# Kernel optimization log

Measured on AMD Instinct MI355X. Metric: run time of the kernel, lower is better.

The kernel has to match this reference:

```python
import jax, jax.numpy as jnp
import numpy as np

B, S, D, H, E, K = 4, 2048, 1024, 2048, 8, 2
GH = max(D // 2, 32)  # 512 gating hidden


def setup_inputs() -> dict:
    key = jax.random.key(0)
    ks = jax.random.split(key, 16)
    def xav(k, shape):
        fan_in, fan_out = shape[0], shape[1]
        lim = (6.0 / (fan_in + fan_out)) ** 0.5
        return jax.random.uniform(k, shape, jnp.float32, -lim, lim)
    return {
        'x': jax.random.normal(ks[0], (B, S, D), jnp.float32),
        'feature_types': jax.random.randint(ks[1], (B, S), 0, 3),
        'gw1': xav(ks[2], (D, GH)), 'gb1': jnp.zeros((GH,), jnp.float32),
        'gw2': xav(ks[3], (GH, GH // 2)), 'gb2': jnp.zeros((GH // 2,), jnp.float32),
        'gw3': xav(ks[4], (GH // 2, E)), 'gb3': jnp.zeros((E,), jnp.float32),
        'type_emb': jax.random.normal(ks[5], (3, GH // 4), jnp.float32),
        'tw': xav(ks[6], (GH // 4, E)), 'tb': jnp.zeros((E,), jnp.float32),
        'ew': jax.random.normal(ks[7], (E, D, H), jnp.float32) * (1.0 / D ** 0.5),
        'eb': jnp.zeros((E, H), jnp.float32),
        'ow': xav(ks[8], (H, D)), 'ob': jnp.zeros((D,), jnp.float32),
    }


def reference(x, feature_types, gw1, gb1, gw2, gb2, gw3, gb3, type_emb, tw, tb, ew, eb, ow, ob):
    # Gating network (eval mode: dropout = identity)
    h = jax.nn.relu(x @ gw1 + gb1)
    h = jax.nn.relu(h @ gw2 + gb2)
    gate_logits = h @ gw3 + gb3                      # [B,S,E]
    type_bias = type_emb[feature_types] @ tw + tb    # [B,S,E]
    gate_weights = jax.nn.softmax(gate_logits + type_bias, axis=-1)

    # Top-k routing, renormalize selected weights
    expert_weights, expert_indices = jax.lax.top_k(gate_weights, K)  # [B,S,K]
    expert_weights = expert_weights / expert_weights.sum(-1, keepdims=True)

    # Dense expert compute (faithful to original: every expert on every token)
    expert_outputs = jnp.einsum('bsd,edh->bseh', x, ew) + eb         # [B,S,E,H]

    # Gather selected experts and combine
    sel = jnp.take_along_axis(expert_outputs, expert_indices[..., None], axis=2)  # [B,S,K,H]
    output = jnp.sum(expert_weights[..., None] * sel, axis=2)        # [B,S,H]

    output = jax.nn.relu(output)
    return output @ ow + ob                                          # [B,S,D]
```

## Files before the change

### kernel.cpp

```cpp
#include <hip/hip_runtime.h>

#define T_TOK 8192
#define DDIM 1024
#define GH1 512
#define GH2 256
#define NEXP 8
#define HDIM 2048

typedef __attribute__((ext_vector_type(8))) short short8;
typedef __attribute__((ext_vector_type(4))) float f32x4;

__device__ __forceinline__ unsigned short f2bf(float f) {
    unsigned int u = __float_as_uint(f);
    u += 0x7fffu + ((u >> 16) & 1u);
    return (unsigned short)(u >> 16);
}
__device__ __forceinline__ float bf2f(unsigned short h) {
    return __uint_as_float(((unsigned int)h) << 16);
}

__device__ __forceinline__ void async16(const void* g, void* l) {
#if __has_builtin(__builtin_amdgcn_global_load_lds)
    __builtin_amdgcn_global_load_lds((const __attribute__((address_space(1))) void*)g,
                                     (__attribute__((address_space(3))) void*)l, 16, 0, 0);
#else
    *(uint4*)l = *(const uint4*)g;
#endif
}

__global__ __launch_bounds__(256)
void f2b_kernel(const float* __restrict__ in, unsigned short* __restrict__ out)
{
    size_t i = ((size_t)blockIdx.x * 256 + threadIdx.x) * 8;
    float4 a = *(const float4*)(in + i);
    float4 b = *(const float4*)(in + i + 4);
    uint4 r;
    r.x = (unsigned)f2bf(a.x) | ((unsigned)f2bf(a.y) << 16);
    r.y = (unsigned)f2bf(a.z) | ((unsigned)f2bf(a.w) << 16);
    r.z = (unsigned)f2bf(b.x) | ((unsigned)f2bf(b.y) << 16);
    r.w = (unsigned)f2bf(b.z) | ((unsigned)f2bf(b.w) << 16);
    *(uint4*)(out + i) = r;
}

__global__ __launch_bounds__(256)
void transpose_f2b(const float* __restrict__ in, unsigned short* __restrict__ out,
                   int R, int C, int tilesC, int ntile)
{
    int bid = blockIdx.x;
    int z = bid / ntile;
    int r = bid - z * ntile;
    int tr = r / tilesC, tc = r - tr * tilesC;
    const float* ib = in + (size_t)z * R * C;
    unsigned short* ob = out + (size_t)z * R * C;
    __shared__ float lds[32][33];
    int t = threadIdx.x;
    int i = t >> 3, j4 = (t & 7) << 2;
    float4 v = *(const float4*)(ib + (size_t)(tr * 32 + i) * C + tc * 32 + j4);
    lds[i][j4 + 0] = v.x;
    lds[i][j4 + 1] = v.y;
    lds[i][j4 + 2] = v.z;
    lds[i][j4 + 3] = v.w;
    __syncthreads();
    ushort4 o;
    o.x = f2bf(lds[j4 + 0][i]);
    o.y = f2bf(lds[j4 + 1][i]);
    o.z = f2bf(lds[j4 + 2][i]);
    o.w = f2bf(lds[j4 + 3][i]);
    *(ushort4*)(ob + (size_t)(tc * 32 + i) * R + tr * 32 + j4) = o;
}

__global__ __launch_bounds__(256)
void sgemm_relu(const float* __restrict__ A, const float* __restrict__ B,
                const float* __restrict__ bias, float* __restrict__ C,
                int N, int Kd, int nbn)
{
    int bid = blockIdx.x;
    int bm = bid / nbn, bn = bid - bm * nbn;
    __shared__ float As[16 * 128];
    __shared__ float Bs[16 * 128];
    int t = threadIdx.x;
    int tx = t & 15, ty = t >> 4;
    float acc[8][8];
#pragma unroll
    for (int i = 0; i < 8; ++i)
#pragma unroll
        for (int j = 0; j < 8; ++j) acc[i][j] = 0.f;

    for (int k0 = 0; k0 < Kd; k0 += 16) {
        __syncthreads();
#pragma unroll
        for (int c = 0; c < 2; ++c) {
            int idx = t + c * 256;
            int row = idx >> 2, kk = (idx & 3) << 2;
            float4 v = *(const float4*)(A + (size_t)(bm * 128 + row) * Kd + k0 + kk);
            As[(kk + 0) * 128 + row] = v.x;
            As[(kk + 1) * 128 + row] = v.y;
            As[(kk + 2) * 128 + row] = v.z;
            As[(kk + 3) * 128 + row] = v.w;
            int kk2 = idx >> 5, n2 = (idx & 31) << 2;
            *(float4*)&Bs[kk2 * 128 + n2] =
                *(const float4*)(B + (size_t)(k0 + kk2) * N + bn * 128 + n2);
        }
        __syncthreads();
#pragma unroll
        for (int kk = 0; kk < 16; ++kk) {
            float a[8], b[8];
            *(float4*)&a[0] = *(const float4*)&As[kk * 128 + ty * 8];
            *(float4*)&a[4] = *(const float4*)&As[kk * 128 + ty * 8 + 4];
            *(float4*)&b[0] = *(const float4*)&Bs[kk * 128 + tx * 8];
            *(float4*)&b[4] = *(const float4*)&Bs[kk * 128 + tx * 8 + 4];
#pragma unroll
            for (int i = 0; i < 8; ++i)
#pragma unroll
                for (int j = 0; j < 8; ++j)
                    acc[i][j] = fmaf(a[i], b[j], acc[i][j]);
        }
    }
#pragma unroll
    for (int i = 0; i < 8; ++i) {
        int row = bm * 128 + ty * 8 + i;
#pragma unroll
        for (int j = 0; j < 8; ++j) {
            int col = bn * 128 + tx * 8 + j;
            float v = acc[i][j] + bias[col];
            C[(size_t)row * N + col] = v > 0.f ? v : 0.f;
        }
    }
}

__global__ __launch_bounds__(256)
void gate_tail(const float* __restrict__ h2, const int* __restrict__ ftyp,
               const float* __restrict__ gw3, const float* __restrict__ gb3,
               const float* __restrict__ temb, const float* __restrict__ tw,
               const float* __restrict__ tb,
               int* __restrict__ eidx, float* __restrict__ ewt)
{
    __shared__ float sw3[GH2 * NEXP];
    __shared__ float stw[128 * NEXP];
    __shared__ float ste[3 * 128];
    int t = threadIdx.x;
    for (int i = t; i < GH2 * NEXP; i += 256) sw3[i] = gw3[i];
    for (int i = t; i < 128 * NEXP; i += 256) stw[i] = tw[i];
    for (int i = t; i < 3 * 128; i += 256) ste[i] = temb[i];
    __syncthreads();
    int tok = blockIdx.x * 256 + t;
    float lg[NEXP];
#pragma unroll
    for (int e = 0; e < NEXP; ++e) lg[e] = gb3[e] + tb[e];
    const float* hrow = h2 + (size_t)tok * GH2;
    for (int k = 0; k < GH2; k += 4) {
        float4 hv = *(const float4*)(hrow + k);
        float hvv[4] = {hv.x, hv.y, hv.z, hv.w};
#pragma unroll
        for (int j = 0; j < 4; ++j) {
            float v = hvv[j];
#pragma unroll
            for (int e = 0; e < NEXP; ++e)
                lg[e] = fmaf(v, sw3[(k + j) * NEXP + e], lg[e]);
        }
    }
    int ft = ftyp[tok];
    const float* te = ste + ft * 128;
    for (int k = 0; k < 128; k += 4) {
#pragma unroll
        for (int j = 0; j < 4; ++j) {
            float v = te[k + j];
#pragma unroll
            for (int e = 0; e < NEXP; ++e)
                lg[e] = fmaf(v, stw[(k + j) * NEXP + e], lg[e]);
        }
    }
    int a0 = 0; float b0 = lg[0];
#pragma unroll
    for (int e = 1; e < NEXP; ++e) if (lg[e] > b0) { b0 = lg[e]; a0 = e; }
    int a1 = -1; float b1 = -3.4e38f;
#pragma unroll
    for (int e = 0; e < NEXP; ++e) if (e != a0 && lg[e] > b1) { b1 = lg[e]; a1 = e; }
    float w0 = 1.f / (1.f + expf(b1 - b0));
    eidx[tok * 2 + 0] = a0;
    eidx[tok * 2 + 1] = a1;
    ewt[tok * 2 + 0] = w0;
    ewt[tok * 2 + 1] = 1.f - w0;
}

__global__ __launch_bounds__(256)
void route_kernel(const int* __restrict__ eidx, int* __restrict__ cnt,
                  int* __restrict__ entries)
{
    int tok = blockIdx.x * 256 + threadIdx.x;
#pragma unroll
    for (int k = 0; k < 2; ++k) {
        int e = eidx[tok * 2 + k];
        int p = atomicAdd(&cnt[e], 1);
        entries[e * T_TOK + p] = (tok << 1) | k;
    }
}

template<int GATHER>
__global__ __launch_bounds__(256)
void bgemm(const unsigned short* __restrict__ A, const unsigned short* __restrict__ BT,
           const float* __restrict__ bias, float* __restrict__ Cf,
           unsigned short* __restrict__ Y0, unsigned short* __restrict__ Y1,
           const int* __restrict__ entries, const int* __restrict__ cnt,
           int N, int Kd, int nbm, int nbn)
{
    int bid = blockIdx.x;
    int e = 0, bm, bn, cntE = 0;
    const unsigned short* Bt = BT;
    const float* bs = bias;
    if (GATHER) {
        e = bid & (NEXP - 1);
        int r = bid >> 3;
        bm = r / nbn; bn = r - bm * nbn;
        cntE = cnt[e];
        if (bm * 128 >= cntE) return;
        Bt = BT + (size_t)e * HDIM * DDIM;
        bs = bias + e * HDIM;
    } else {
        bm = bid / nbn; bn = bid - bm * nbn;
    }

    __shared__ __align__(16) unsigned short As[128 * 32];
    __shared__ __align__(16) unsigned short Bs[128 * 32];
    __shared__ int rowtok[128];

    int t = threadIdx.x;
    if (GATHER) {
        if (t < 128) {
            int idx = bm * 128 + t;
            rowtok[t] = entries[(size_t)e * T_TOK + bm * 128 + ((idx < cntE) ? t : 0)];
        }
        __syncthreads();
    }

    int arow0 = t >> 2;
    int kkA = (t & 3) << 3;
    const unsigned short *asrc0, *asrc1;
    if (GATHER) {
        asrc0 = A + (size_t)(rowtok[arow0] >> 1) * Kd + kkA;
        asrc1 = A + (size_t)(rowtok[arow0 + 64] >> 1) * Kd + kkA;
    } else {
        asrc0 = A + (size_t)(bm * 128 + arow0) * Kd + kkA;
        asrc1 = A + (size_t)(bm * 128 + arow0 + 64) * Kd + kkA;
    }
    const unsigned short* bsrc0 = Bt + (size_t)(bn * 128 + arow0) * Kd + kkA;
    const unsigned short* bsrc1 = Bt + (size_t)(bn * 128 + arow0 + 64) * Kd + kkA;
    unsigned short* adst0 = As + t * 8;
    unsigned short* adst1 = As + t * 8 + 2048;
    unsigned short* bdst0 = Bs + t * 8;
    unsigned short* bdst1 = Bs + t * 8 + 2048;

    int lane = t & 63, wave = t >> 6;
    int wr = (wave >> 1) * 64, wc = (wave & 1) * 64;
    int l15 = lane & 15, lhi = lane >> 4;

    f32x4 zero = {0.f, 0.f, 0.f, 0.f};
    f32x4 acc[4][4];
#pragma unroll
    for (int m = 0; m < 4; ++m)
#pragma unroll
        for (int n = 0; n < 4; ++n) acc[m][n] = zero;

    for (int k0 = 0; k0 < Kd; k0 += 32) {
        __syncthreads();
        async16(asrc0 + k0, adst0);
        async16(asrc1 + k0, adst1);
        async16(bsrc0 + k0, bdst0);
        async16(bsrc1 + k0, bdst1);
        __syncthreads();
        short8 af[4], bf[4];
#pragma unroll
        for (int m = 0; m < 4; ++m)
            af[m] = *(const short8*)&As[(wr + m * 16 + l15) * 32 + lhi * 8];
#pragma unroll
        for (int n = 0; n < 4; ++n)
            bf[n] = *(const short8*)&Bs[(wc + n * 16 + l15) * 32 + lhi * 8];
#pragma unroll
        for (int m = 0; m < 4; ++m)
#pragma unroll
            for (int n = 0; n < 4; ++n)
                acc[m][n] = __builtin_amdgcn_mfma_f32_16x16x32_bf16(af[m], bf[n], acc[m][n], 0, 0, 0);
    }

    if (GATHER) {
#pragma unroll
        for (int m = 0; m < 4; ++m) {
            int rl = wr + m * 16 + lhi * 4;
#pragma unroll
            for (int q = 0; q < 4; ++q) {
                int gidx = bm * 128 + rl + q;
                if (gidx < cntE) {
                    int ent = rowtok[rl + q];
                    unsigned short* Y = (ent & 1) ? Y1 : Y0;
                    size_t rowoff = (size_t)(ent >> 1) * HDIM;
#pragma unroll
                    for (int n = 0; n < 4; ++n) {
                        int col = bn * 128 + wc + n * 16 + l15;
                        Y[rowoff + col] = f2bf(acc[m][n][q] + bs[col]);
                    }
                }
            }
        }
    } else {
#pragma unroll
        for (int m = 0; m < 4; ++m) {
            int row = bm * 128 + wr + m * 16 + lhi * 4;
#pragma unroll
            for (int n = 0; n < 4; ++n) {
                int col = bn * 128 + wc + n * 16 + l15;
                float bv = bs[col];
#pragma unroll
                for (int q = 0; q < 4; ++q)
                    Cf[(size_t)(row + q) * N + col] = acc[m][n][q] + bv;
            }
        }
    }
}

__global__ __launch_bounds__(256)
void combine_kernel(const unsigned short* __restrict__ Y0,
                    const unsigned short* __restrict__ Y1,
                    const float* __restrict__ wts,
                    unsigned short* __restrict__ Hc)
{
    size_t i = (size_t)blockIdx.x * 256 + threadIdx.x;
    size_t base = i * 8;
    int tok = (int)(base >> 11);
    float w0 = wts[tok * 2], w1 = wts[tok * 2 + 1];
    uint4 a = *(const uint4*)(Y0 + base);
    uint4 b = *(const uint4*)(Y1 + base);
    unsigned int ain[4] = {a.x, a.y, a.z, a.w};
    unsigned int bin[4] = {b.x, b.y, b.z, b.w};
    unsigned int r[4];
#pragma unroll
    for (int q = 0; q < 4; ++q) {
        float v0 = w0 * bf2f((unsigned short)(ain[q] & 0xffff)) +
                   w1 * bf2f((unsigned short)(bin[q] & 0xffff));
        float v1 = w0 * bf2f((unsigned short)(ain[q] >> 16)) +
                   w1 * bf2f((unsigned short)(bin[q] >> 16));
        v0 = v0 > 0.f ? v0 : 0.f;
        v1 = v1 > 0.f ? v1 : 0.f;
        r[q] = (unsigned int)f2bf(v0) | ((unsigned int)f2bf(v1) << 16);
    }
    uint4 o = {r[0], r[1], r[2], r[3]};
    *(uint4*)(Hc + base) = o;
}

extern "C" void kernel_launch(void* const* d_in, const int* in_sizes, int n_in,
                              void* d_out, int out_size, void* d_ws, size_t ws_size,
                              hipStream_t stream)
{
    const float* x    = (const float*)d_in[0];
    const int*   ftyp = (const int*)d_in[1];
    const float* gw1  = (const float*)d_in[2];
    const float* gb1  = (const float*)d_in[3];
    const float* gw2  = (const float*)d_in[4];
    const float* gb2  = (const float*)d_in[5];
    const float* gw3  = (const float*)d_in[6];
    const float* gb3  = (const float*)d_in[7];
    const float* temb = (const float*)d_in[8];
    const float* tw   = (const float*)d_in[9];
    const float* tb   = (const float*)d_in[10];
    const float* ew   = (const float*)d_in[11];
    const float* eb   = (const float*)d_in[12];
    const float* ow   = (const float*)d_in[13];
    const float* ob   = (const float*)d_in[14];
    float* out = (float*)d_out;

    char* p = (char*)d_ws;
    auto alloc = [&](size_t bytes) {
        char* r = p;
        p += (bytes + 255) & ~(size_t)255;
        return r;
    };
    unsigned short* xb  = (unsigned short*)alloc((size_t)T_TOK * DDIM * 2);
    float* h1           = (float*)alloc((size_t)T_TOK * GH1 * 4);
    float* h2           = (float*)alloc((size_t)T_TOK * GH2 * 4);
    int* eidx           = (int*)alloc((size_t)T_TOK * 2 * 4);
    float* ewt          = (float*)alloc((size_t)T_TOK * 2 * 4);
    int* cnt            = (int*)alloc(256);
    int* entries        = (int*)alloc((size_t)NEXP * T_TOK * 4);
    unsigned short* ewT = (unsigned short*)alloc((size_t)NEXP * HDIM * DDIM * 2);
    unsigned short* owT = (unsigned short*)alloc((size_t)DDIM * HDIM * 2);
    unsigned short* Y0  = (unsigned short*)alloc((size_t)T_TOK * HDIM * 2);
    unsigned short* Y1  = (unsigned short*)alloc((size_t)T_TOK * HDIM * 2);
    unsigned short* Hc  = (unsigned short*)alloc((size_t)T_TOK * HDIM * 2);

    hipMemsetAsync(cnt, 0, 256, stream);
    f2b_kernel<<<(T_TOK * DDIM / 8) / 256, 256, 0, stream>>>(x, xb);
    transpose_f2b<<<NEXP * 32 * 64, 256, 0, stream>>>(ew, ewT, DDIM, HDIM, 64, 32 * 64);
    transpose_f2b<<<64 * 32, 256, 0, stream>>>(ow, owT, HDIM, DDIM, 32, 64 * 32);

    sgemm_relu<<<64 * 4, 256, 0, stream>>>(x, gw1, gb1, h1, GH1, DDIM, 4);
    sgemm_relu<<<64 * 2, 256, 0, stream>>>(h1, gw2, gb2, h2, GH2, GH1, 2);
    gate_tail<<<T_TOK / 256, 256, 0, stream>>>(h2, ftyp, gw3, gb3, temb, tw, tb, eidx, ewt);
    route_kernel<<<T_TOK / 256, 256, 0, stream>>>(eidx, cnt, entries);

    bgemm<1><<<NEXP * 64 * 16, 256, 0, stream>>>(xb, ewT, eb, nullptr, Y0, Y1,
                                                 entries, cnt, HDIM, DDIM, 64, 16);
    combine_kernel<<<(T_TOK * HDIM / 8) / 256, 256, 0, stream>>>(Y0, Y1, ewt, Hc);
    bgemm<0><<<64 * 8, 256, 0, stream>>>(Hc, owT, ob, out, nullptr, nullptr,
                                         nullptr, nullptr, DDIM, HDIM, 64, 8);
}
```

Measured before the change: 746.4 us.

## Double-buffer bf16 GEMM LDS tiles and shrink gating SGEMM tiles for occupancy

The MFMA bgemm now double-buffers its A/B LDS tiles, issuing the async global-to-LDS loads for the next K-step before computing on the current one and dropping one barrier per iteration. This is meant to hide load latency behind the MFMAs, at the cost of doubled LDS use per block. The fp32 gating SGEMM goes from 128x128 to 64x64 tiles with 4x4 per-thread accumulators, register-prefetched global loads and vectorised stores. That launches 4x more blocks so the small gating GEMMs fill the GPU better, though each block does less reuse.

```diff
diff --git a/kernel.cpp b/kernel.cpp
--- a/kernel.cpp
+++ b/kernel.cpp
@@ -76,55 +76,55 @@
 {
     int bid = blockIdx.x;
     int bm = bid / nbn, bn = bid - bm * nbn;
-    __shared__ float As[16 * 128];
-    __shared__ float Bs[16 * 128];
+    __shared__ float As[16][64];
+    __shared__ float Bs[16][64];
     int t = threadIdx.x;
     int tx = t & 15, ty = t >> 4;
-    float acc[8][8];
-#pragma unroll
-    for (int i = 0; i < 8; ++i)
-#pragma unroll
-        for (int j = 0; j < 8; ++j) acc[i][j] = 0.f;
+    float acc[4][4];
+#pragma unroll
+    for (int i = 0; i < 4; ++i)
+#pragma unroll
+        for (int j = 0; j < 4; ++j) acc[i][j] = 0.f;
+
+    int arow = t >> 2, akk = (t & 3) << 2;
+    int bkk = t >> 4, bcol = (t & 15) << 2;
+    const float* aptr = A + (size_t)(bm * 64 + arow) * Kd + akk;
+    const float* bptr = B + (size_t)bkk * N + bn * 64 + bcol;
 
     for (int k0 = 0; k0 < Kd; k0 += 16) {
+        float4 av = *(const float4*)(aptr + k0);
+        float4 bv = *(const float4*)(bptr + (size_t)k0 * N);
         __syncthreads();
-#pragma unroll
-        for (int c = 0; c < 2; ++c) {
-            int idx = t + c * 256;
-            int row = idx >> 2, kk = (idx & 3) << 2;
-            float4 v = *(const float4*)(A + (size_t)(bm * 128 + row) * Kd + k0 + kk);
-            As[(kk + 0) * 128 + row] = v.x;
-            As[(kk + 1) * 128 + row] = v.y;
-            As[(kk + 2) * 128 + row] = v.z;
-            As[(kk + 3) * 128 + row] = v.w;
-            int kk2 = idx >> 5, n2 = (idx & 31) << 2;
-            *(float4*)&Bs[kk2 * 128 + n2] =
-                *(const float4*)(B + (size_t)(k0 + kk2) * N + bn * 128 + n2);
-        }
+        As[akk + 0][arow] = av.x;
+        As[akk + 1][arow] = av.y;
+        As[akk + 2][arow] = av.z;
+        As[akk + 3][arow] = av.w;
+        *(float4*)&Bs[bkk][bcol] = bv;
         __syncthreads();
 #pragma unroll
         for (int kk = 0; kk < 16; ++kk) {
-            float a[8], b[8];
-            *(float4*)&a[0] = *(const float4*)&As[kk * 128 + ty * 8];
-            *(float4*)&a[4] = *(const float4*)&As[kk * 128 + ty * 8 + 4];
-            *(float4*)&b[0] = *(const float4*)&Bs[kk * 128 + tx * 8];
-            *(float4*)&b[4] = *(const float4*)&Bs[kk * 128 + tx * 8 + 4];
-#pragma unroll
-            for (int i = 0; i < 8; ++i)
-#pragma unroll
-                for (int j = 0; j < 8; ++j)
+            float a[4], b[4];
+            *(float4*)&a[0] = *(const float4*)&As[kk][ty * 4];
+            *(float4*)&b[0] = *(const float4*)&Bs[kk][tx * 4];
+#pragma unroll
+            for (int i = 0; i < 4; ++i)
+#pragma unroll
+                for (int j = 0; j < 4; ++j)
                     acc[i][j] = fmaf(a[i], b[j], acc[i][j]);
         }
     }
 #pragma unroll
-    for (int i = 0; i < 8; ++i) {
-        int row = bm * 128 + ty * 8 + i;
-#pragma unroll
-        for (int j = 0; j < 8; ++j) {
-            int col = bn * 128 + tx * 8 + j;
+    for (int i = 0; i < 4; ++i) {
+        int row = bm * 64 + ty * 4 + i;
+        float4 o;
+        float* op = &o.x;
+#pragma unroll
+        for (int j = 0; j < 4; ++j) {
+            int col = bn * 64 + tx * 4 + j;
             float v = acc[i][j] + bias[col];
-            C[(size_t)row * N + col] = v > 0.f ? v : 0.f;
-        }
+            op[j] = v > 0.f ? v : 0.f;
+        }
+        *(float4*)&C[(size_t)row * N + bn * 64 + tx * 4] = o;
     }
 }
 
@@ -220,8 +220,8 @@
         bm = bid / nbn; bn = bid - bm * nbn;
     }
 
-    __shared__ __align__(16) unsigned short As[128 * 32];
-    __shared__ __align__(16) unsigned short Bs[128 * 32];
+    __shared__ __align__(16) unsigned short As[2][128 * 32];
+    __shared__ __align__(16) unsigned short Bs[2][128 * 32];
     __shared__ int rowtok[128];
 
     int t = threadIdx.x;
@@ -245,10 +245,6 @@
     }
     const unsigned short* bsrc0 = Bt + (size_t)(bn * 128 + arow0) * Kd + kkA;
     const unsigned short* bsrc1 = Bt + (size_t)(bn * 128 + arow0 + 64) * Kd + kkA;
-    unsigned short* adst0 = As + t * 8;
-    unsigned short* adst1 = As + t * 8 + 2048;
-    unsigned short* bdst0 = Bs + t * 8;
-    unsigned short* bdst1 = Bs + t * 8 + 2048;
 
     int lane = t & 63, wave = t >> 6;
     int wr = (wave >> 1) * 64, wc = (wave & 1) * 64;
@@ -261,25 +257,37 @@
 #pragma unroll
         for (int n = 0; n < 4; ++n) acc[m][n] = zero;
 
-    for (int k0 = 0; k0 < Kd; k0 += 32) {
-        __syncthreads();
-        async16(asrc0 + k0, adst0);
-        async16(asrc1 + k0, adst1);
-        async16(bsrc0 + k0, bdst0);
-        async16(bsrc1 + k0, bdst1);
-        __syncthreads();
+    async16(asrc0, &As[0][t * 8]);
+    async16(asrc1, &As[0][t * 8 + 2048]);
+    async16(bsrc0, &Bs[0][t * 8]);
+    async16(bsrc1, &Bs[0][t * 8 + 2048]);
+    __syncthreads();
+
+    int nt = Kd >> 5;
+    int cur = 0;
+    for (int kt = 0; kt < nt; ++kt) {
+        if (kt + 1 < nt) {
+            int k0 = (kt + 1) << 5;
+            int nb = cur ^ 1;
+            async16(asrc0 + k0, &As[nb][t * 8]);
+            async16(asrc1 + k0, &As[nb][t * 8 + 2048]);
+            async16(bsrc0 + k0, &Bs[nb][t * 8]);
+            async16(bsrc1 + k0, &Bs[nb][t * 8 + 2048]);
+        }
         short8 af[4], bf[4];
 #pragma unroll
         for (int m = 0; m < 4; ++m)
-            af[m] = *(const short8*)&As[(wr + m * 16 + l15) * 32 + lhi * 8];
+            af[m] = *(const short8*)&As[cur][(wr + m * 16 + l15) * 32 + lhi * 8];
 #pragma unroll
         for (int n = 0; n < 4; ++n)
-            bf[n] = *(const short8*)&Bs[(wc + n * 16 + l15) * 32 + lhi * 8];
+            bf[n] = *(const short8*)&Bs[cur][(wc + n * 16 + l15) * 32 + lhi * 8];
 #pragma unroll
         for (int m = 0; m < 4; ++m)
 #pragma unroll
             for (int n = 0; n < 4; ++n)
                 acc[m][n] = __builtin_amdgcn_mfma_f32_16x16x32_bf16(af[m], bf[n], acc[m][n], 0, 0, 0);
+        __syncthreads();
+        cur ^= 1;
     }
 
     if (GATHER) {
@@ -391,8 +399,8 @@
     transpose_f2b<<<NEXP * 32 * 64, 256, 0, stream>>>(ew, ewT, DDIM, HDIM, 64, 32 * 64);
     transpose_f2b<<<64 * 32, 256, 0, stream>>>(ow, owT, HDIM, DDIM, 32, 64 * 32);
 
-    sgemm_relu<<<64 * 4, 256, 0, stream>>>(x, gw1, gb1, h1, GH1, DDIM, 4);
-    sgemm_relu<<<64 * 2, 256, 0, stream>>>(h1, gw2, gb2, h2, GH2, GH1, 2);
+    sgemm_relu<<<128 * 8, 256, 0, stream>>>(x, gw1, gb1, h1, GH1, DDIM, 8);
+    sgemm_relu<<<128 * 4, 256, 0, stream>>>(h1, gw2, gb2, h2, GH2, GH1, 4);
     gate_tail<<<T_TOK / 256, 256, 0, stream>>>(h2, ftyp, gw3, gb3, temb, tw, tb, eidx, ewt);
     route_kernel<<<T_TOK / 256, 256, 0, stream>>>(eidx, cnt, entries);
 
```

After: 670.5 us. 1.11x faster.
